# Performance work log

Hardware: AMD Instinct MI355X
Metric: run time of the kernel (lower is better)

The kernel has to match this reference:

```python
import jax, jax.numpy as jnp
import numpy as np

NUM_NEIGHBORS = 3
EPS = 1e-10
B, N1, N2 = 8, 8192, 2048
C1, C2 = 256, 512


def setup_inputs() -> dict:
    key = jax.random.key(0)
    k1, k2, k3, k4 = jax.random.split(key, 4)
    return {
        "query_xyz": jax.random.uniform(k1, (B, 3, N1), dtype=jnp.float32),
        "key_xyz": jax.random.uniform(k2, (B, 3, N2), dtype=jnp.float32),
        "query_feature": jax.random.normal(k3, (B, C1, N1), dtype=jnp.float32),
        "key_feature": jax.random.normal(k4, (B, C2, N2), dtype=jnp.float32),
    }


def reference(query_xyz, key_xyz, query_feature, key_feature):
    # q: (B, N1, 3), k: (B, N2, 3)
    q = jnp.swapaxes(query_xyz, 1, 2)
    k = jnp.swapaxes(key_xyz, 1, 2)
    # squared pairwise distances (B, N1, N2) via ||q||^2 + ||k||^2 - 2 q.k
    d2 = (
        jnp.sum(q * q, axis=-1, keepdims=True)
        + jnp.sum(k * k, axis=-1)[:, None, :]
        - 2.0 * jnp.einsum("bnd,bmd->bnm", q, k)
    )
    # k nearest neighbors (smallest distances)
    neg_d, index = jax.lax.top_k(-d2, NUM_NEIGHBORS)  # (B, N1, K)
    distance = jnp.maximum(-neg_d, EPS)
    inv_distance = 1.0 / distance
    weight = inv_distance / jnp.sum(inv_distance, axis=2, keepdims=True)
    # torch.no_grad() block -> constants w.r.t. autodiff
    weight = jax.lax.stop_gradient(weight)
    index = jax.lax.stop_gradient(index)
    # gather key features: feat_t (B, N2, C2) -> gathered (B, N1, K, C2)
    feat_t = jnp.swapaxes(key_feature, 1, 2)
    batch_idx = jnp.arange(feat_t.shape[0])[:, None, None]
    gathered = feat_t[batch_idx, index]
    # inverse-distance weighted sum -> (B, C2, N1)
    interpolated = jnp.einsum("bnk,bnkc->bcn", weight, gathered)
    return jnp.concatenate([interpolated, query_feature], axis=1)
```

## Files before the change

kernel.cpp:

```cpp
#include <hip/hip_runtime.h>

#define NB 8
#define N1 8192
#define N2 2048
#define C1 256
#define C2 512
#define CO 768
#define CCH 4


#define NRM2(X, Y, Z) ({                                                   \
    float _s, _t;                                                          \
    asm("v_mul_f32 %0, %2, %2\n\t"                                         \
        "v_mul_f32 %1, %3, %3\n\t"                                         \
        "v_add_f32 %0, %0, %1\n\t"                                         \
        "v_mul_f32 %1, %4, %4\n\t"                                         \
        "v_add_f32 %0, %0, %1"                                             \
        : "=&v"(_s), "=&v"(_t) : "v"(X), "v"(Y), "v"(Z));                  \
    _s; })

#define D2PIN(QX, QY, QZ, QQ, X, Y, Z, KK) ({                              \
    float _d, _t;                                                          \
    asm("v_mul_f32 %0, %2, %5\n\t"             \
        "v_fma_f32 %0, %3, %6, %0\n\t"         \
        "v_fma_f32 %0, %4, %7, %0\n\t"         \
        "v_add_f32 %1, %8, %9\n\t"             \
        "v_mul_f32 %0, 2.0, %0\n\t"            \
        "v_sub_f32 %0, %1, %0"                 \
        : "=&v"(_d), "=&v"(_t)                                             \
        : "v"(QX), "v"(QY), "v"(QZ), "v"(X), "v"(Y), "v"(Z),               \
          "v"(QQ), "v"(KK));                                               \
    _d; })

__global__ __launch_bounds__(256, 4) void knn_fused(
    const float* __restrict__ qxyz,
    const float* __restrict__ kxyz,
    int*   __restrict__ nn_idx,
    float* __restrict__ nn_w)
{
    __shared__ __align__(16) float skx[N2];
    __shared__ __align__(16) float sky[N2];
    __shared__ __align__(16) float skz[N2];
    __shared__ __align__(16) float skk[N2];
    __shared__ float pd[4][64][3];
    __shared__ int   pi[4][64][3];

    const int b   = blockIdx.x >> 7;
    const int n0  = (blockIdx.x & 127) * 64;
    const int tid = threadIdx.x;
    const int w   = tid >> 6, lane = tid & 63;

    const float* kb = kxyz + (size_t)b * 3 * N2;
    for (int j = tid; j < N2; j += 256) {
        float x = kb[j], y = kb[N2 + j], z = kb[2 * N2 + j];
        skx[j] = x; sky[j] = y; skz[j] = z;
        skk[j] = NRM2(x, y, z);
    }
    __syncthreads();

    const int n = n0 + lane;
    const float* qb = qxyz + (size_t)b * 3 * N1;
    const float qx = qb[n], qy = qb[N1 + n], qz = qb[2 * N1 + n];
    const float qq = NRM2(qx, qy, qz);

    float b0 = 3.4e38f, b1 = 3.4e38f, b2 = 3.4e38f;
    int   i0 = 0, i1 = 0, i2 = 0;

#define PROC(X, Y, Z, KK, J) do {                                          \
        float d2 = D2PIN(qx, qy, qz, qq, (X), (Y), (Z), (KK));             \
        if (d2 < b2) {                                                     \
            bool c0 = d2 < b0, c1 = d2 < b1;                               \
            b2 = c1 ? b1 : d2;               i2 = c1 ? i1 : (J);           \
            b1 = c0 ? b0 : (c1 ? d2 : b1);   i1 = c0 ? i0 : (c1 ? (J) : i1); \
            b0 = c0 ? d2 : b0;               i0 = c0 ? (J) : i0;           \
        }                                                                  \
    } while (0)

    const int jlo = w * (N2 / 4), jhi = jlo + (N2 / 4);
    #pragma unroll 4
    for (int jb = jlo; jb < jhi; jb += 4) {
        float4 x4 = *(const float4*)&skx[jb];
        float4 y4 = *(const float4*)&sky[jb];
        float4 z4 = *(const float4*)&skz[jb];
        float4 k4 = *(const float4*)&skk[jb];
        PROC(x4.x, y4.x, z4.x, k4.x, jb + 0);
        PROC(x4.y, y4.y, z4.y, k4.y, jb + 1);
        PROC(x4.z, y4.z, z4.z, k4.z, jb + 2);
        PROC(x4.w, y4.w, z4.w, k4.w, jb + 3);
    }
#undef PROC

    pd[w][lane][0] = b0; pd[w][lane][1] = b1; pd[w][lane][2] = b2;
    pi[w][lane][0] = i0; pi[w][lane][1] = i1; pi[w][lane][2] = i2;
    __syncthreads();

    if (tid < 64) {
        float m0 = 3.4e38f, m1 = 3.4e38f, m2 = 3.4e38f;
        int   j0 = 0, j1 = 0, j2 = 0;
        #pragma unroll
        for (int c = 0; c < 4; ++c) {
            #pragma unroll
            for (int s = 0; s < 3; ++s) {
                float d = pd[c][tid][s];
                int   i = pi[c][tid][s];
                if (d < m2) {
                    bool c0 = d < m0, c1 = d < m1;
                    m2 = c1 ? m1 : d;                j2 = c1 ? j1 : i;
                    m1 = c0 ? m0 : (c1 ? d : m1);    j1 = c0 ? j0 : (c1 ? i : j1);
                    m0 = c0 ? d : m0;                j0 = c0 ? i  : j0;
                }
            }
        }
        float d0f = fmaxf(m0, 1e-10f), d1f = fmaxf(m1, 1e-10f), d2f = fmaxf(m2, 1e-10f);
        float v0 = __fdiv_rn(1.0f, d0f), v1 = __fdiv_rn(1.0f, d1f), v2 = __fdiv_rn(1.0f, d2f);
        float s  = __fadd_rn(__fadd_rn(v0, v1), v2);
        const size_t g = (size_t)b * N1 + n0 + tid;
        int4   iv = make_int4(j0, j1, j2, 0);
        float4 wv = make_float4(__fdiv_rn(v0, s), __fdiv_rn(v1, s),
                                __fdiv_rn(v2, s), 0.0f);
        *(int4*)  &nn_idx[g * 4] = iv;
        *(float4*)&nn_w  [g * 4] = wv;
    }
}

__global__ __launch_bounds__(256) void interp4(
    const float* __restrict__ kfeat,
    const int*   __restrict__ nn_idx,
    const float* __restrict__ nn_w,
    const float* __restrict__ qfeat,
    float* __restrict__ out)
{
    __shared__ __align__(16) float4 skf[N2];
    const int b     = blockIdx.x & 7;
    const int cg    = blockIdx.x >> 3;
    const int cbase = cg * CCH;
    const int tid   = threadIdx.x;

    const float* kf = kfeat + (size_t)b * C2 * N2 + (size_t)cbase * N2;
    for (int j = tid; j < N2; j += 256) {
        skf[j] = make_float4(kf[j], kf[N2 + j], kf[2 * N2 + j], kf[3 * N2 + j]);
    }
    __syncthreads();

    const int*   ib = nn_idx + (size_t)b * N1 * 4;
    const float* wb = nn_w   + (size_t)b * N1 * 4;
    float* ob = out + (size_t)b * CO * N1;

    #pragma unroll 4
    for (int t = 0; t < N1 / 256; ++t) {
        const int n = t * 256 + tid;
        const int4   iv = *(const int4*)  &ib[(size_t)n * 4];
        const float4 wv = *(const float4*)&wb[(size_t)n * 4];
        const float4 f0 = skf[iv.x];
        const float4 f1 = skf[iv.y];
        const float4 f2 = skf[iv.z];
        ob[(size_t)(cbase + 0) * N1 + n] =
            fmaf(wv.z, f2.x, fmaf(wv.y, f1.x, __fmul_rn(wv.x, f0.x)));
        ob[(size_t)(cbase + 1) * N1 + n] =
            fmaf(wv.z, f2.y, fmaf(wv.y, f1.y, __fmul_rn(wv.x, f0.y)));
        ob[(size_t)(cbase + 2) * N1 + n] =
            fmaf(wv.z, f2.z, fmaf(wv.y, f1.z, __fmul_rn(wv.x, f0.z)));
        ob[(size_t)(cbase + 3) * N1 + n] =
            fmaf(wv.z, f2.w, fmaf(wv.y, f1.w, __fmul_rn(wv.x, f0.w)));
    }

    const float4* qsrc = (const float4*)(qfeat + (size_t)b * C1 * N1);
    float4*       qdst = (float4*)(out + (size_t)b * CO * N1 + (size_t)C2 * N1);
    #pragma unroll
    for (int k = 0; k < 16; ++k) {
        const size_t r = (size_t)cg * 4096 + (size_t)k * 256 + tid;
        qdst[r] = qsrc[r];
    }
}

extern "C" void kernel_launch(void* const* d_in, const int* in_sizes, int n_in,
                              void* d_out, int out_size, void* d_ws, size_t ws_size,
                              hipStream_t stream) {
    const float* qxyz  = (const float*)d_in[0];
    const float* kxyz  = (const float*)d_in[1];
    const float* qfeat = (const float*)d_in[2];
    const float* kfeat = (const float*)d_in[3];
    float* out = (float*)d_out;

    int*   nn_idx = (int*)d_ws;
    float* nn_w   = (float*)d_ws + (size_t)4 * NB * N1;

    knn_fused<<<NB * (N1 / 64), 256, 0, stream>>>(qxyz, kxyz, nn_idx, nn_w);
    interp4<<<NB * (C2 / CCH), 256, 0, stream>>>(kfeat, nn_idx, nn_w, qfeat, out);
}
```

Measured before the change: 116.0 us.

## Pack keys once and scan them via scalar loads, move qfeat copy into KNN

A new pre-pass packs key xyz plus squared norm into float4s in workspace. The KNN kernel then reads keys straight from global memory with wave-uniform loads that feed SGPR operands into the distance asm, instead of staging them in LDS. The block grows to 8 waves, each scanning N2/8 keys, and the query-feature copy moves from the interp kernel into the KNN kernel. This removes per-block LDS staging and its barrier and lets the copy overlap with compute, at the cost of an extra launch and a larger merge step.

```diff
diff --git a/kernel.cpp b/kernel.cpp
--- a/kernel.cpp
+++ b/kernel.cpp
@@ -19,44 +19,46 @@
         : "=&v"(_s), "=&v"(_t) : "v"(X), "v"(Y), "v"(Z));                  \
     _s; })
 
-#define D2PIN(QX, QY, QZ, QQ, X, Y, Z, KK) ({                              \
+#define D2PIN_S(QX, QY, QZ, QQ, SX, SY, SZ, SKK) ({                        \
     float _d, _t;                                                          \
-    asm("v_mul_f32 %0, %2, %5\n\t"             \
-        "v_fma_f32 %0, %3, %6, %0\n\t"         \
-        "v_fma_f32 %0, %4, %7, %0\n\t"         \
-        "v_add_f32 %1, %8, %9\n\t"             \
+    asm("v_mul_f32 %0, %5, %2\n\t"             \
+        "v_fma_f32 %0, %6, %3, %0\n\t"         \
+        "v_fma_f32 %0, %7, %4, %0\n\t"         \
+        "v_add_f32 %1, %9, %8\n\t"             \
         "v_mul_f32 %0, 2.0, %0\n\t"            \
         "v_sub_f32 %0, %1, %0"                 \
         : "=&v"(_d), "=&v"(_t)                                             \
-        : "v"(QX), "v"(QY), "v"(QZ), "v"(X), "v"(Y), "v"(Z),               \
-          "v"(QQ), "v"(KK));                                               \
+        : "v"(QX), "v"(QY), "v"(QZ), "s"(SX), "s"(SY), "s"(SZ),            \
+          "v"(QQ), "s"(SKK));                                              \
     _d; })
 
-__global__ __launch_bounds__(256, 4) void knn_fused(
+__global__ __launch_bounds__(256) void pack_keys(
+    const float* __restrict__ kxyz,
+    float4* __restrict__ keys4)
+{
+    const int b = blockIdx.x >> 3;
+    const int j = (blockIdx.x & 7) * 256 + threadIdx.x;
+    const float* kb = kxyz + (size_t)b * 3 * N2;
+    float x = kb[j], y = kb[N2 + j], z = kb[2 * N2 + j];
+    keys4[(size_t)b * N2 + j] = make_float4(x, y, z, NRM2(x, y, z));
+}
+
+__global__ __launch_bounds__(512) void knn_scan(
     const float* __restrict__ qxyz,
-    const float* __restrict__ kxyz,
+    const float4* __restrict__ keys4,
+    const float* __restrict__ qfeat,
     int*   __restrict__ nn_idx,
-    float* __restrict__ nn_w)
+    float* __restrict__ nn_w,
+    float* __restrict__ out)
 {
-    __shared__ __align__(16) float skx[N2];
-    __shared__ __align__(16) float sky[N2];
-    __shared__ __align__(16) float skz[N2];
-    __shared__ __align__(16) float skk[N2];
-    __shared__ float pd[4][64][3];
-    __shared__ int   pi[4][64][3];
+    __shared__ float pd[8][64][3];
+    __shared__ int   pi[8][64][3];
 
-    const int b   = blockIdx.x >> 7;
-    const int n0  = (blockIdx.x & 127) * 64;
-    const int tid = threadIdx.x;
-    const int w   = tid >> 6, lane = tid & 63;
-
-    const float* kb = kxyz + (size_t)b * 3 * N2;
-    for (int j = tid; j < N2; j += 256) {
-        float x = kb[j], y = kb[N2 + j], z = kb[2 * N2 + j];
-        skx[j] = x; sky[j] = y; skz[j] = z;
-        skk[j] = NRM2(x, y, z);
-    }
-    __syncthreads();
+    const int b    = blockIdx.x >> 7;
+    const int tile = blockIdx.x & 127;
+    const int n0   = tile * 64;
+    const int tid  = threadIdx.x;
+    const int w    = tid >> 6, lane = tid & 63;
 
     const int n = n0 + lane;
     const float* qb = qxyz + (size_t)b * 3 * N1;
@@ -67,7 +69,7 @@
     int   i0 = 0, i1 = 0, i2 = 0;
 
 #define PROC(X, Y, Z, KK, J) do {                                          \
-        float d2 = D2PIN(qx, qy, qz, qq, (X), (Y), (Z), (KK));             \
+        float d2 = D2PIN_S(qx, qy, qz, qq, (X), (Y), (Z), (KK));           \
         if (d2 < b2) {                                                     \
             bool c0 = d2 < b0, c1 = d2 < b1;                               \
             b2 = c1 ? b1 : d2;               i2 = c1 ? i1 : (J);           \
@@ -76,17 +78,12 @@
         }                                                                  \
     } while (0)
 
-    const int jlo = w * (N2 / 4), jhi = jlo + (N2 / 4);
-    #pragma unroll 4
-    for (int jb = jlo; jb < jhi; jb += 4) {
-        float4 x4 = *(const float4*)&skx[jb];
-        float4 y4 = *(const float4*)&sky[jb];
-        float4 z4 = *(const float4*)&skz[jb];
-        float4 k4 = *(const float4*)&skk[jb];
-        PROC(x4.x, y4.x, z4.x, k4.x, jb + 0);
-        PROC(x4.y, y4.y, z4.y, k4.y, jb + 1);
-        PROC(x4.z, y4.z, z4.z, k4.z, jb + 2);
-        PROC(x4.w, y4.w, z4.w, k4.w, jb + 3);
+    const float4* kb4 = keys4 + (size_t)b * N2;
+    const int jlo = w * (N2 / 8);
+    #pragma unroll 8
+    for (int u = 0; u < N2 / 8; ++u) {
+        const float4 k4 = kb4[jlo + u];
+        PROC(k4.x, k4.y, k4.z, k4.w, jlo + u);
     }
 #undef PROC
 
@@ -98,7 +95,7 @@
         float m0 = 3.4e38f, m1 = 3.4e38f, m2 = 3.4e38f;
         int   j0 = 0, j1 = 0, j2 = 0;
         #pragma unroll
-        for (int c = 0; c < 4; ++c) {
+        for (int c = 0; c < 8; ++c) {
             #pragma unroll
             for (int s = 0; s < 3; ++s) {
                 float d = pd[c][tid][s];
@@ -115,11 +112,17 @@
         float v0 = __fdiv_rn(1.0f, d0f), v1 = __fdiv_rn(1.0f, d1f), v2 = __fdiv_rn(1.0f, d2f);
         float s  = __fadd_rn(__fadd_rn(v0, v1), v2);
         const size_t g = (size_t)b * N1 + n0 + tid;
-        int4   iv = make_int4(j0, j1, j2, 0);
-        float4 wv = make_float4(__fdiv_rn(v0, s), __fdiv_rn(v1, s),
-                                __fdiv_rn(v2, s), 0.0f);
-        *(int4*)  &nn_idx[g * 4] = iv;
-        *(float4*)&nn_w  [g * 4] = wv;
+        *(int4*)  &nn_idx[g * 4] = make_int4(j0, j1, j2, 0);
+        *(float4*)&nn_w  [g * 4] = make_float4(__fdiv_rn(v0, s), __fdiv_rn(v1, s),
+                                               __fdiv_rn(v2, s), 0.0f);
+    }
+
+    const float4* qsrc = (const float4*)(qfeat + (size_t)b * C1 * N1);
+    float4*       qdst = (float4*)(out + (size_t)b * CO * N1 + (size_t)C2 * N1);
+    #pragma unroll
+    for (int k = 0; k < 8; ++k) {
+        const size_t r = (size_t)tile * 4096 + (size_t)k * 512 + tid;
+        qdst[r] = qsrc[r];
     }
 }
 
@@ -127,7 +130,6 @@
     const float* __restrict__ kfeat,
     const int*   __restrict__ nn_idx,
     const float* __restrict__ nn_w,
-    const float* __restrict__ qfeat,
     float* __restrict__ out)
 {
     __shared__ __align__(16) float4 skf[N2];
@@ -163,14 +165,6 @@
         ob[(size_t)(cbase + 3) * N1 + n] =
             fmaf(wv.z, f2.w, fmaf(wv.y, f1.w, __fmul_rn(wv.x, f0.w)));
     }
-
-    const float4* qsrc = (const float4*)(qfeat + (size_t)b * C1 * N1);
-    float4*       qdst = (float4*)(out + (size_t)b * CO * N1 + (size_t)C2 * N1);
-    #pragma unroll
-    for (int k = 0; k < 16; ++k) {
-        const size_t r = (size_t)cg * 4096 + (size_t)k * 256 + tid;
-        qdst[r] = qsrc[r];
-    }
 }
 
 extern "C" void kernel_launch(void* const* d_in, const int* in_sizes, int n_in,
@@ -182,9 +176,13 @@
     const float* kfeat = (const float*)d_in[3];
     float* out = (float*)d_out;
 
-    int*   nn_idx = (int*)d_ws;
-    float* nn_w   = (float*)d_ws + (size_t)4 * NB * N1;
+    float*  ws     = (float*)d_ws;
+    float4* keys4  = (float4*)ws;
+    int*    nn_idx = (int*)(ws + (size_t)4 * NB * N2);
+    float*  nn_w   = ws + (size_t)4 * NB * N2 + (size_t)4 * NB * N1;
 
-    knn_fused<<<NB * (N1 / 64), 256, 0, stream>>>(qxyz, kxyz, nn_idx, nn_w);
-    interp4<<<NB * (C2 / CCH), 256, 0, stream>>>(kfeat, nn_idx, nn_w, qfeat, out);
+    pack_keys<<<NB * (N2 / 256), 256, 0, stream>>>(kxyz, keys4);
+    knn_scan<<<NB * (N1 / 64), 512, 0, stream>>>(qxyz, keys4, qfeat,
+                                                 nn_idx, nn_w, out);
+    interp4<<<NB * (C2 / CCH), 256, 0, stream>>>(kfeat, nn_idx, nn_w, out);
 }
```

Result: slower. 132.1 us (+13.9%).
